# Performance work log

Measured on AMD Instinct MI355X. Metric: run time of the kernel, lower is better.

## Reference

```python
import jax, jax.numpy as jnp
import numpy as np

EMBED_DIM = 1024
NUM_HEADS = 16
HEAD_DIM = EMBED_DIM // NUM_HEADS
EPS = 1e-6


def setup_inputs() -> dict:
    key = jax.random.key(0)
    ks = jax.random.split(key, 10)
    B, S, D = 4, 2048, EMBED_DIM
    def xavier(k, shape):
        fan_in, fan_out = shape[1], shape[0]
        limit = float(np.sqrt(6.0 / (fan_in + fan_out)))
        return jax.random.uniform(k, shape, jnp.float32, -limit, limit)
    return {
        "x": jax.random.normal(ks[0], (B, S, D), jnp.float32),
        "ln_gamma": jnp.ones((D,), jnp.float32),
        "ln_beta": jnp.zeros((D,), jnp.float32),
        "Wq": xavier(ks[1], (D, D)), "bq": jnp.zeros((D,), jnp.float32),
        "Wk": xavier(ks[2], (D, D)), "bk": jnp.zeros((D,), jnp.float32),
        "Wv": xavier(ks[3], (D, D)), "bv": jnp.zeros((D,), jnp.float32),
        "Wo": xavier(ks[4], (D, D)), "bo": jnp.zeros((D,), jnp.float32),
    }


def reference(x, ln_gamma, ln_beta, Wq, bq, Wk, bk, Wv, bv, Wo, bo):
    B, S, D = x.shape
    # Pre-LayerNorm
    mu = jnp.mean(x, axis=-1, keepdims=True)
    var = jnp.mean((x - mu) ** 2, axis=-1, keepdims=True)
    xn = (x - mu) / jnp.sqrt(var + EPS) * ln_gamma + ln_beta
    # QKV projections (torch Linear: y = x @ W.T + b)
    def split_heads(t):  # [B,S,D] -> [B,H,S,hd]
        return t.reshape(B, S, NUM_HEADS, HEAD_DIM).transpose(0, 2, 1, 3)
    q = split_heads(xn @ Wq.T + bq)
    k = split_heads(xn @ Wk.T + bk)
    v = split_heads(xn @ Wv.T + bv)
    scale = 1.0 / jnp.sqrt(jnp.float32(HEAD_DIM))
    scores = jnp.einsum("bhqd,bhkd->bhqk", q, k) * scale
    probs = jax.nn.softmax(scores, axis=-1)  # dropout is identity (eval)
    ctx = jnp.einsum("bhqk,bhkd->bhqd", probs, v)
    ctx = ctx.transpose(0, 2, 1, 3).reshape(B, S, D)
    out = ctx @ Wo.T + bo  # proj dropout identity (eval)
    return out
```

## Files before the change

### kernel.cpp

```cpp
#include <hip/hip_runtime.h>
#include <hip/hip_bf16.h>
#include <stdint.h>

typedef __bf16 bf16x8 __attribute__((ext_vector_type(8)));
typedef short short8 __attribute__((ext_vector_type(8)));
typedef float f32x4 __attribute__((ext_vector_type(4)));

#define LOG2E 1.44269504088896340736f

__device__ inline void gload_lds16(const void* g, void* l) {
  __builtin_amdgcn_global_load_lds((const __attribute__((address_space(1))) void*)g,
                                   (__attribute__((address_space(3))) void*)l, 16, 0, 0);
}

__device__ inline unsigned short bf16_bits(float f) {
  return __builtin_bit_cast(unsigned short, __float2bfloat16(f));
}

__device__ inline float fast_exp2(float x) {
  return __builtin_amdgcn_exp2f(x);
}

__device__ inline uint32_t cvtpk_bf16(float lo, float hi) {
  uint32_t d;
  asm("v_cvt_pk_bf16_f32 %0, %1, %2" : "=v"(d) : "v"(lo), "v"(hi));
  return d;
}
__device__ inline void plswap32(uint32_t& a, uint32_t& b) {
  asm("v_permlane32_swap_b32 %0, %1" : "+v"(a), "+v"(b));
}
__device__ inline void plswap16(uint32_t& a, uint32_t& b) {
  asm("v_permlane16_swap_b32 %0, %1" : "+v"(a), "+v"(b));
}

__global__ __launch_bounds__(256) void prep_kernel(
    const float* __restrict__ x, const float* __restrict__ gamma,
    const float* __restrict__ beta, __hip_bfloat16* __restrict__ xn,
    const float* __restrict__ Wq, const float* __restrict__ Wk,
    const float* __restrict__ Wv, const float* __restrict__ Wo,
    __hip_bfloat16* __restrict__ Wqk, __hip_bfloat16* __restrict__ Wvb,
    __hip_bfloat16* __restrict__ Wob)
{
  const int t = threadIdx.x;
  if (blockIdx.x < 8192) {
    const int row = blockIdx.x;
    const float4 v = reinterpret_cast<const float4*>(x + (size_t)row * 1024)[t];
    float s = v.x + v.y + v.z + v.w;
    float q = v.x*v.x + v.y*v.y + v.z*v.z + v.w*v.w;
    #pragma unroll
    for (int off = 32; off >= 1; off >>= 1) {
      s += __shfl_xor(s, off);
      q += __shfl_xor(q, off);
    }
    __shared__ float ls[4], lq[4];
    const int wave = t >> 6, lane = t & 63;
    if (lane == 0) { ls[wave] = s; lq[wave] = q; }
    __syncthreads();
    s = ls[0] + ls[1] + ls[2] + ls[3];
    q = lq[0] + lq[1] + lq[2] + lq[3];
    const float mean = s * (1.0f/1024.0f);
    const float var  = q * (1.0f/1024.0f) - mean*mean;
    const float rstd = rsqrtf(var + 1e-6f);
    const float4 gm = reinterpret_cast<const float4*>(gamma)[t];
    const float4 bt = reinterpret_cast<const float4*>(beta)[t];
    ushort4 o;
    o.x = bf16_bits((v.x - mean)*rstd*gm.x + bt.x);
    o.y = bf16_bits((v.y - mean)*rstd*gm.y + bt.y);
    o.z = bf16_bits((v.z - mean)*rstd*gm.z + bt.z);
    o.w = bf16_bits((v.w - mean)*rstd*gm.w + bt.w);
    reinterpret_cast<ushort4*>(xn + (size_t)row*1024)[t] = o;
  } else {
    const int cb = blockIdx.x - 8192;
    const int which = cb >> 10;
    const int i = (cb & 1023) * 256 + t;
    const float* src;
    __hip_bfloat16* dst;
    if (which == 0)      { src = Wq; dst = Wqk; }
    else if (which == 1) { src = Wk; dst = Wqk + 1024*1024; }
    else if (which == 2) { src = Wv; dst = Wvb; }
    else                 { src = Wo; dst = Wob; }
    const float4 v = reinterpret_cast<const float4*>(src)[i];
    ushort4 o;
    o.x = bf16_bits(v.x); o.y = bf16_bits(v.y);
    o.z = bf16_bits(v.z); o.w = bf16_bits(v.w);
    reinterpret_cast<ushort4*>(dst)[i] = o;
  }
}

template<int MODE>
__device__ __forceinline__ void gemm_body(
    const __hip_bfloat16* __restrict__ A,
    const __hip_bfloat16* __restrict__ B,
    int m0, int n0,
    const float* __restrict__ bias0,
    const float* __restrict__ bias1,
    void* __restrict__ C0,
    void* __restrict__ C1,
    __hip_bfloat16* Al, __hip_bfloat16* Bl)
{
  constexpr int K = 1024;
  const int t = threadIdx.x;
  const int wave = t >> 6, lane = t & 63;
  const int li = lane & 15, g = lane >> 4;
  const int wm = (wave >> 1) * 64, wn = (wave & 1) * 64;

  const int srow = t >> 3;
  const int scb_e = ((((t & 7) * 16) ^ ((srow & 7) << 4)) >> 1);
  const __hip_bfloat16* ga = A + (size_t)(m0 + srow) * K + scb_e;
  const __hip_bfloat16* gb = B + (size_t)(n0 + srow) * K + scb_e;

  const int swz = (li & 7) << 4;
  const int rd0 = (((g*16)      ^ swz) >> 1);
  const int rd1 = (((g*16 + 64) ^ swz) >> 1);

  f32x4 acc[4][4] = {};

  for (int kt = 0; kt < K; kt += 64) {
    #pragma unroll
    for (int i = 0; i < 4; ++i) {
      gload_lds16(ga + (size_t)(i*32)*K + kt, Al + i*2048 + t*8);
      gload_lds16(gb + (size_t)(i*32)*K + kt, Bl + i*2048 + t*8);
    }
    __syncthreads();
    bf16x8 af[4][2], bfr[4][2];
    #pragma unroll
    for (int mi = 0; mi < 4; ++mi) {
      af[mi][0] = *reinterpret_cast<const bf16x8*>(&Al[(wm + mi*16 + li)*64 + rd0]);
      af[mi][1] = *reinterpret_cast<const bf16x8*>(&Al[(wm + mi*16 + li)*64 + rd1]);
    }
    #pragma unroll
    for (int ni = 0; ni < 4; ++ni) {
      bfr[ni][0] = *reinterpret_cast<const bf16x8*>(&Bl[(wn + ni*16 + li)*64 + rd0]);
      bfr[ni][1] = *reinterpret_cast<const bf16x8*>(&Bl[(wn + ni*16 + li)*64 + rd1]);
    }
    __builtin_amdgcn_s_setprio(1);
    #pragma unroll
    for (int mi = 0; mi < 4; ++mi)
      #pragma unroll
      for (int ni = 0; ni < 4; ++ni) {
        acc[mi][ni] = __builtin_amdgcn_mfma_f32_16x16x32_bf16(af[mi][0], bfr[ni][0], acc[mi][ni], 0, 0, 0);
        acc[mi][ni] = __builtin_amdgcn_mfma_f32_16x16x32_bf16(af[mi][1], bfr[ni][1], acc[mi][ni], 0, 0, 0);
      }
    __builtin_amdgcn_s_setprio(0);
    __syncthreads();
  }

  #pragma unroll
  for (int mi = 0; mi < 4; ++mi) {
    #pragma unroll
    for (int ni = 0; ni < 4; ++ni) {
      #pragma unroll
      for (int r = 0; r < 4; ++r) {
        const int grow = m0 + wm + mi*16 + g*4 + r;
        const int gcol = n0 + wn + ni*16 + li;
        float v = acc[mi][ni][r];
        if constexpr (MODE == 0) {
          const int b = grow >> 11, ss = grow & 2047;
          if (gcol < 1024) {
            v = (v + bias0[gcol]) * (0.125f * LOG2E);
            const int h = gcol >> 6, d = gcol & 63;
            ((__hip_bfloat16*)C0)[(((size_t)(b*16 + h))*2048 + ss)*64 + d] = __float2bfloat16(v);
          } else {
            const int c2 = gcol - 1024;
            v = v + bias1[c2];
            const int h = c2 >> 6, d = c2 & 63;
            ((__hip_bfloat16*)C1)[(((size_t)(b*16 + h))*2048 + ss)*64 + d] = __float2bfloat16(v);
          }
        } else if constexpr (MODE == 1) {
          v += bias0[grow];
          ((__hip_bfloat16*)C0)[(size_t)grow*8192 + gcol] = __float2bfloat16(v);
        } else {
          v += bias0[gcol];
          ((float*)C0)[(size_t)grow*1024 + gcol] = v;
        }
      }
    }
  }
}

__global__ __launch_bounds__(256) void qkv_gemm(
    const __hip_bfloat16* __restrict__ xn,
    const __hip_bfloat16* __restrict__ Wqk,
    const __hip_bfloat16* __restrict__ Wvb,
    const float* __restrict__ bq, const float* __restrict__ bk,
    const float* __restrict__ bv,
    __hip_bfloat16* __restrict__ Qb, __hip_bfloat16* __restrict__ Kb,
    __hip_bfloat16* __restrict__ Vt)
{
  __shared__ __align__(16) __hip_bfloat16 Al[128*64];
  __shared__ __align__(16) __hip_bfloat16 Bl[128*64];
  const int lin = blockIdx.x;
  const int wg  = (lin & 7) * 192 + (lin >> 3);
  if (wg < 1024) {
    const int m0 = (wg >> 4) * 128, n0 = (wg & 15) * 128;
    gemm_body<0>(xn, Wqk, m0, n0, bq, bk, Qb, Kb, Al, Bl);
  } else {
    const int w2 = wg - 1024;
    const int m0 = (w2 & 7) * 128, n0 = (w2 >> 3) * 128;
    gemm_body<1>(Wvb, xn, m0, n0, bv, nullptr, Vt, nullptr, Al, Bl);
  }
}

__global__ __launch_bounds__(256) void out_gemm(
    const __hip_bfloat16* __restrict__ A,
    const __hip_bfloat16* __restrict__ B,
    const float* __restrict__ bias,
    float* __restrict__ C)
{
  __shared__ __align__(16) __hip_bfloat16 Al[128*64];
  __shared__ __align__(16) __hip_bfloat16 Bl[128*64];
  const int lin = blockIdx.x;
  const int wg  = (lin & 7) * 64 + (lin >> 3);
  const int m0 = (wg >> 3) * 128, n0 = (wg & 7) * 128;
  gemm_body<2>(A, B, m0, n0, bias, nullptr, C, nullptr, Al, Bl);
}

__global__ __launch_bounds__(512, 8) void attn_kernel(
    const __hip_bfloat16* __restrict__ Q,
    const __hip_bfloat16* __restrict__ K,
    const __hip_bfloat16* __restrict__ Vt,
    __hip_bfloat16* __restrict__ ctx)
{
  const int t = threadIdx.x, wave = t >> 6, lane = t & 63;
  const int li = lane & 15, g = lane >> 4;

  const int lin = blockIdx.x;
  const int wg  = (lin & 7) * 128 + (lin >> 3);
  const int bh  = wg >> 4, qt = wg & 15;
  const int b = bh >> 4, h = bh & 15;
  const int qbase = qt * 128 + wave * 16;

  __shared__ __align__(16) __hip_bfloat16 Klds[2][4096];
  __shared__ __align__(16) __hip_bfloat16 Vlds[2][4096];

  const bf16x8* Qv = reinterpret_cast<const bf16x8*>(Q + ((size_t)bh*2048 + qbase + li)*64 + g*8);
  const bf16x8 aQ0 = Qv[0], aQ1 = Qv[4];

  const short8 ones_s = { 0x3F80, 0x3F80, 0x3F80, 0x3F80, 0x3F80, 0x3F80, 0x3F80, 0x3F80 };
  const bf16x8 ones = __builtin_bit_cast(bf16x8, ones_s);

  f32x4 acc[4] = {};
  f32x4 acc_l = {};

  const __hip_bfloat16* Kbh = K + (size_t)bh*2048*64;
  const __hip_bfloat16* Vbh = Vt + (size_t)h*64*8192 + b*2048;

  const int row0 = t >> 3;
  const int scb_e = ((((t & 7) * 16) ^ ((row0 & 7) << 4)) >> 1);

  const int krd0 = (li*128 + ((g*16)      ^ ((li & 7) << 4))) >> 1;
  const int krd1 = (li*128 + ((g*16 + 64) ^ ((li & 7) << 4))) >> 1;

  gload_lds16(Kbh + (size_t)row0*64 + scb_e,        &Klds[0][t*8]);
  gload_lds16(Vbh + (size_t)row0*8192 + scb_e,      &Vlds[0][t*8]);
  gload_lds16(Kbh + (size_t)(64+row0)*64 + scb_e,   &Klds[1][t*8]);
  gload_lds16(Vbh + (size_t)row0*8192 + 64 + scb_e, &Vlds[1][t*8]);
  asm volatile("s_waitcnt vmcnt(2)" ::: "memory");
  __builtin_amdgcn_sched_barrier(0);
  __builtin_amdgcn_s_barrier();

  const __hip_bfloat16* kSrc = Kbh + (size_t)(128 + row0)*64 + scb_e;
  const __hip_bfloat16* vSrc = Vbh + (size_t)row0*8192 + 128 + scb_e;

  for (int it = 0; it < 32; ++it) {
    const int cur = it & 1;
    const __hip_bfloat16* Kc = Klds[cur];
    const __hip_bfloat16* Vc = Vlds[cur];

    f32x4 s[4] = {};
    __builtin_amdgcn_s_setprio(1);
    #pragma unroll
    for (int nt = 0; nt < 4; ++nt) {
      const bf16x8 k0 = *reinterpret_cast<const bf16x8*>(&Kc[nt*1024 + krd0]);
      const bf16x8 k1 = *reinterpret_cast<const bf16x8*>(&Kc[nt*1024 + krd1]);
      s[nt] = __builtin_amdgcn_mfma_f32_16x16x32_bf16(k0, aQ0, s[nt], 0, 0, 0);
      s[nt] = __builtin_amdgcn_mfma_f32_16x16x32_bf16(k1, aQ1, s[nt], 0, 0, 0);
    }
    __builtin_amdgcn_s_setprio(0);

    #pragma unroll
    for (int nt = 0; nt < 4; ++nt)
      #pragma unroll
      for (int r = 0; r < 4; ++r)
        s[nt][r] = fast_exp2(s[nt][r]);

    union U8 { uint32_t w[4]; bf16x8 v; };
    bf16x8 aP0, aP1;
    {
      uint32_t c[4][2];
      #pragma unroll
      for (int nt = 0; nt < 4; ++nt) {
        c[nt][0] = cvtpk_bf16(s[nt][0], s[nt][1]);
        c[nt][1] = cvtpk_bf16(s[nt][2], s[nt][3]);
      }
      uint32_t x0 = c[0][0], y0 = c[1][0], x1 = c[0][1], y1 = c[1][1];
      plswap32(x0, y0); plswap32(x1, y1);
      plswap16(x0, y0); plswap16(x1, y1);
      U8 u0; u0.w[0] = x0; u0.w[1] = x1; u0.w[2] = y0; u0.w[3] = y1;
      aP0 = u0.v;
      uint32_t x2 = c[2][0], y2 = c[3][0], x3 = c[2][1], y3 = c[3][1];
      plswap32(x2, y2); plswap32(x3, y3);
      plswap16(x2, y2); plswap16(x3, y3);
      U8 u1; u1.w[0] = x2; u1.w[1] = x3; u1.w[2] = y2; u1.w[3] = y3;
      aP1 = u1.v;
    }

    __builtin_amdgcn_s_setprio(1);
    #pragma unroll
    for (int dt = 0; dt < 4; ++dt) {
      const bf16x8 v0 = *reinterpret_cast<const bf16x8*>(&Vc[dt*1024 + krd0]);
      const bf16x8 v1 = *reinterpret_cast<const bf16x8*>(&Vc[dt*1024 + krd1]);
      acc[dt] = __builtin_amdgcn_mfma_f32_16x16x32_bf16(v0, aP0, acc[dt], 0, 0, 0);
      acc[dt] = __builtin_amdgcn_mfma_f32_16x16x32_bf16(v1, aP1, acc[dt], 0, 0, 0);
    }
    acc_l = __builtin_amdgcn_mfma_f32_16x16x32_bf16(ones, aP0, acc_l, 0, 0, 0);
    acc_l = __builtin_amdgcn_mfma_f32_16x16x32_bf16(ones, aP1, acc_l, 0, 0, 0);
    __builtin_amdgcn_s_setprio(0);

    if (it < 31) {
      __builtin_amdgcn_s_barrier();
      if (it < 30) {
        gload_lds16(kSrc, &Klds[cur][t*8]);
        gload_lds16(vSrc, &Vlds[cur][t*8]);
        kSrc += 64*64;
        vSrc += 64;
        asm volatile("s_waitcnt vmcnt(2)" ::: "memory");
      } else {
        asm volatile("s_waitcnt vmcnt(0)" ::: "memory");
      }
      __builtin_amdgcn_sched_barrier(0);
      __builtin_amdgcn_s_barrier();
    }
  }

  const float inv = 1.0f / acc_l[0];

  __hip_bfloat16* cp = ctx + ((size_t)(b*2048 + qbase))*1024 + h*64;
  #pragma unroll
  for (int dt = 0; dt < 4; ++dt) {
    ushort4 o;
    o.x = bf16_bits(acc[dt][0] * inv);
    o.y = bf16_bits(acc[dt][1] * inv);
    o.z = bf16_bits(acc[dt][2] * inv);
    o.w = bf16_bits(acc[dt][3] * inv);
    *reinterpret_cast<ushort4*>(&cp[(size_t)li*1024 + dt*16 + g*4]) = o;
  }
}

extern "C" void kernel_launch(void* const* d_in, const int* in_sizes, int n_in,
                              void* d_out, int out_size, void* d_ws, size_t ws_size,
                              hipStream_t stream)
{
  const float* x  = (const float*)d_in[0];
  const float* g  = (const float*)d_in[1];
  const float* be = (const float*)d_in[2];
  const float* Wq = (const float*)d_in[3];
  const float* bq = (const float*)d_in[4];
  const float* Wk = (const float*)d_in[5];
  const float* bk = (const float*)d_in[6];
  const float* Wv = (const float*)d_in[7];
  const float* bv = (const float*)d_in[8];
  const float* Wo = (const float*)d_in[9];
  const float* bo = (const float*)d_in[10];
  float* out = (float*)d_out;

  char* ws = (char*)d_ws;
  __hip_bfloat16* xn  = (__hip_bfloat16*)(ws);
  __hip_bfloat16* Wqk = (__hip_bfloat16*)(ws + 16777216);
  __hip_bfloat16* Wvb = (__hip_bfloat16*)(ws + 20971520);
  __hip_bfloat16* Wob = (__hip_bfloat16*)(ws + 23068672);
  __hip_bfloat16* Qb  = (__hip_bfloat16*)(ws + 25165824);
  __hip_bfloat16* Kb  = (__hip_bfloat16*)(ws + 41943040);
  __hip_bfloat16* Vt  = (__hip_bfloat16*)(ws + 58720256);
  __hip_bfloat16* ctx = (__hip_bfloat16*)(ws + 75497472);

  prep_kernel<<<12288, 256, 0, stream>>>(x, g, be, xn, Wq, Wk, Wv, Wo, Wqk, Wvb, Wob);
  qkv_gemm<<<1536, 256, 0, stream>>>(xn, Wqk, Wvb, bq, bk, bv, Qb, Kb, Vt);
  attn_kernel<<<1024, 512, 0, stream>>>(Qb, Kb, Vt, ctx);
  out_gemm<<<512, 256, 0, stream>>>(ctx, Wob, bo, out);
}
```

Baseline: 189.0 us.

## Use 64x128 thin GEMM tiles for V and output projections; unroll attention loop

Adds a thin GEMM body with 64-row tiles (each wave covers 64x32) for the V projection and the output projection. This doubles the number of workgroups (1536 to 2048 for QKV, 512 to 1024 for the output GEMM) to fill the GPU's compute units better. The attention main loop is manually unrolled by two so the double-buffer index and branches become compile-time constant. Smaller tiles lower per-block arithmetic intensity and increase global/LDS traffic.

Measured after the change: 224.1 us. 18.6% more time.

```diff
diff --git a/kernel.cpp b/kernel.cpp
--- a/kernel.cpp
+++ b/kernel.cpp
@@ -87,15 +87,12 @@
   }
 }
 
-template<int MODE>
-__device__ __forceinline__ void gemm_body(
+__device__ __forceinline__ void gemm_body128(
     const __hip_bfloat16* __restrict__ A,
     const __hip_bfloat16* __restrict__ B,
     int m0, int n0,
-    const float* __restrict__ bias0,
-    const float* __restrict__ bias1,
-    void* __restrict__ C0,
-    void* __restrict__ C1,
+    const float* __restrict__ bq, const float* __restrict__ bk,
+    __hip_bfloat16* __restrict__ Qb, __hip_bfloat16* __restrict__ Kb,
     __hip_bfloat16* Al, __hip_bfloat16* Bl)
 {
   constexpr int K = 1024;
@@ -154,24 +151,94 @@
         const int grow = m0 + wm + mi*16 + g*4 + r;
         const int gcol = n0 + wn + ni*16 + li;
         float v = acc[mi][ni][r];
-        if constexpr (MODE == 0) {
-          const int b = grow >> 11, ss = grow & 2047;
-          if (gcol < 1024) {
-            v = (v + bias0[gcol]) * (0.125f * LOG2E);
-            const int h = gcol >> 6, d = gcol & 63;
-            ((__hip_bfloat16*)C0)[(((size_t)(b*16 + h))*2048 + ss)*64 + d] = __float2bfloat16(v);
-          } else {
-            const int c2 = gcol - 1024;
-            v = v + bias1[c2];
-            const int h = c2 >> 6, d = c2 & 63;
-            ((__hip_bfloat16*)C1)[(((size_t)(b*16 + h))*2048 + ss)*64 + d] = __float2bfloat16(v);
-          }
-        } else if constexpr (MODE == 1) {
-          v += bias0[grow];
-          ((__hip_bfloat16*)C0)[(size_t)grow*8192 + gcol] = __float2bfloat16(v);
+        const int b = grow >> 11, ss = grow & 2047;
+        if (gcol < 1024) {
+          v = (v + bq[gcol]) * (0.125f * LOG2E);
+          const int h = gcol >> 6, d = gcol & 63;
+          Qb[(((size_t)(b*16 + h))*2048 + ss)*64 + d] = __float2bfloat16(v);
         } else {
-          v += bias0[gcol];
-          ((float*)C0)[(size_t)grow*1024 + gcol] = v;
+          const int c2 = gcol - 1024;
+          v = v + bk[c2];
+          const int h = c2 >> 6, d = c2 & 63;
+          Kb[(((size_t)(b*16 + h))*2048 + ss)*64 + d] = __float2bfloat16(v);
+        }
+      }
+    }
+  }
+}
+
+template<int MODE>
+__device__ __forceinline__ void gemm_body_thin(
+    const __hip_bfloat16* __restrict__ A,
+    const __hip_bfloat16* __restrict__ B,
+    int m0, int n0,
+    const float* __restrict__ bias,
+    void* __restrict__ C,
+    __hip_bfloat16* Al, __hip_bfloat16* Bl)
+{
+  constexpr int K = 1024;
+  const int t = threadIdx.x;
+  const int wave = t >> 6, lane = t & 63;
+  const int li = lane & 15, g = lane >> 4;
+  const int wn = wave * 32;
+
+  const int srow = t >> 3;
+  const int scb_e = ((((t & 7) * 16) ^ ((srow & 7) << 4)) >> 1);
+  const __hip_bfloat16* ga = A + (size_t)(m0 + srow) * K + scb_e;
+  const __hip_bfloat16* gb = B + (size_t)(n0 + srow) * K + scb_e;
+
+  const int swz = (li & 7) << 4;
+  const int rd0 = (((g*16)      ^ swz) >> 1);
+  const int rd1 = (((g*16 + 64) ^ swz) >> 1);
+
+  f32x4 acc[4][2] = {};
+
+  for (int kt = 0; kt < K; kt += 64) {
+    #pragma unroll
+    for (int i = 0; i < 2; ++i)
+      gload_lds16(ga + (size_t)(i*32)*K + kt, Al + i*2048 + t*8);
+    #pragma unroll
+    for (int i = 0; i < 4; ++i)
+      gload_lds16(gb + (size_t)(i*32)*K + kt, Bl + i*2048 + t*8);
+    __syncthreads();
+    bf16x8 af[4][2], bfr[2][2];
+    #pragma unroll
+    for (int mi = 0; mi < 4; ++mi) {
+      af[mi][0] = *reinterpret_cast<const bf16x8*>(&Al[(mi*16 + li)*64 + rd0]);
+      af[mi][1] = *reinterpret_cast<const bf16x8*>(&Al[(mi*16 + li)*64 + rd1]);
+    }
+    #pragma unroll
+    for (int ni = 0; ni < 2; ++ni) {
+      bfr[ni][0] = *reinterpret_cast<const bf16x8*>(&Bl[(wn + ni*16 + li)*64 + rd0]);
+      bfr[ni][1] = *reinterpret_cast<const bf16x8*>(&Bl[(wn + ni*16 + li)*64 + rd1]);
+    }
+    __builtin_amdgcn_s_setprio(1);
+    #pragma unroll
+    for (int mi = 0; mi < 4; ++mi)
+      #pragma unroll
+      for (int ni = 0; ni < 2; ++ni) {
+        acc[mi][ni] = __builtin_amdgcn_mfma_f32_16x16x32_bf16(af[mi][0], bfr[ni][0], acc[mi][ni], 0, 0, 0);
+        acc[mi][ni] = __builtin_amdgcn_mfma_f32_16x16x32_bf16(af[mi][1], bfr[ni][1], acc[mi][ni], 0, 0, 0);
+      }
+    __builtin_amdgcn_s_setprio(0);
+    __syncthreads();
+  }
+
+  #pragma unroll
+  for (int mi = 0; mi < 4; ++mi) {
+    #pragma unroll
+    for (int ni = 0; ni < 2; ++ni) {
+      #pragma unroll
+      for (int r = 0; r < 4; ++r) {
+        const int grow = m0 + mi*16 + g*4 + r;
+        const int gcol = n0 + wn + ni*16 + li;
+        float v = acc[mi][ni][r];
+        if constexpr (MODE == 1) {
+          v += bias[grow];
+          ((__hip_bfloat16*)C)[(size_t)grow*8192 + gcol] = __float2bfloat16(v);
+        } else {
+          v += bias[gcol];
+          ((float*)C)[(size_t)grow*1024 + gcol] = v;
         }
       }
     }
@@ -190,14 +257,14 @@
   __shared__ __align__(16) __hip_bfloat16 Al[128*64];
   __shared__ __align__(16) __hip_bfloat16 Bl[128*64];
   const int lin = blockIdx.x;
-  const int wg  = (lin & 7) * 192 + (lin >> 3);
+  const int wg  = (lin & 7) * 256 + (lin >> 3);
   if (wg < 1024) {
     const int m0 = (wg >> 4) * 128, n0 = (wg & 15) * 128;
-    gemm_body<0>(xn, Wqk, m0, n0, bq, bk, Qb, Kb, Al, Bl);
+    gemm_body128(xn, Wqk, m0, n0, bq, bk, Qb, Kb, Al, Bl);
   } else {
     const int w2 = wg - 1024;
-    const int m0 = (w2 & 7) * 128, n0 = (w2 >> 3) * 128;
-    gemm_body<1>(Wvb, xn, m0, n0, bv, nullptr, Vt, nullptr, Al, Bl);
+    const int m0 = (w2 >> 6) * 64, n0 = (w2 & 63) * 128;
+    gemm_body_thin<1>(Wvb, xn, m0, n0, bv, Vt, Al, Bl);
   }
 }
 
@@ -207,12 +274,12 @@
     const float* __restrict__ bias,
     float* __restrict__ C)
 {
-  __shared__ __align__(16) __hip_bfloat16 Al[128*64];
+  __shared__ __align__(16) __hip_bfloat16 Al[64*64];
   __shared__ __align__(16) __hip_bfloat16 Bl[128*64];
   const int lin = blockIdx.x;
-  const int wg  = (lin & 7) * 64 + (lin >> 3);
-  const int m0 = (wg >> 3) * 128, n0 = (wg & 7) * 128;
-  gemm_body<2>(A, B, m0, n0, bias, nullptr, C, nullptr, Al, Bl);
+  const int wg  = (lin & 7) * 128 + (lin >> 3);
+  const int m0 = (wg >> 3) * 64, n0 = (wg & 7) * 128;
+  gemm_body_thin<2>(A, B, m0, n0, bias, C, Al, Bl);
 }
 
 __global__ __launch_bounds__(512, 8) void attn_kernel(
@@ -251,22 +318,7 @@
   const int krd0 = (li*128 + ((g*16)      ^ ((li & 7) << 4))) >> 1;
   const int krd1 = (li*128 + ((g*16 + 64) ^ ((li & 7) << 4))) >> 1;
 
-  gload_lds16(Kbh + (size_t)row0*64 + scb_e,        &Klds[0][t*8]);
-  gload_lds16(Vbh + (size_t)row0*8192 + scb_e,      &Vlds[0][t*8]);
-  gload_lds16(Kbh + (size_t)(64+row0)*64 + scb_e,   &Klds[1][t*8]);
-  gload_lds16(Vbh + (size_t)row0*8192 + 64 + scb_e, &Vlds[1][t*8]);
-  asm volatile("s_waitcnt vmcnt(2)" ::: "memory");
-  __builtin_amdgcn_sched_barrier(0);
-  __builtin_amdgcn_s_barrier();
-
-  const __hip_bfloat16* kSrc = Kbh + (size_t)(128 + row0)*64 + scb_e;
-  const __hip_bfloat16* vSrc = Vbh + (size_t)row0*8192 + 128 + scb_e;
-
-  for (int it = 0; it < 32; ++it) {
-    const int cur = it & 1;
-    const __hip_bfloat16* Kc = Klds[cur];
-    const __hip_bfloat16* Vc = Vlds[cur];
-
+  auto compute = [&](const __hip_bfloat16* Kc, const __hip_bfloat16* Vc) {
     f32x4 s[4] = {};
     __builtin_amdgcn_s_setprio(1);
     #pragma unroll
@@ -316,22 +368,43 @@
     acc_l = __builtin_amdgcn_mfma_f32_16x16x32_bf16(ones, aP0, acc_l, 0, 0, 0);
     acc_l = __builtin_amdgcn_mfma_f32_16x16x32_bf16(ones, aP1, acc_l, 0, 0, 0);
     __builtin_amdgcn_s_setprio(0);
-
-    if (it < 31) {
-      __builtin_amdgcn_s_barrier();
-      if (it < 30) {
-        gload_lds16(kSrc, &Klds[cur][t*8]);
-        gload_lds16(vSrc, &Vlds[cur][t*8]);
-        kSrc += 64*64;
-        vSrc += 64;
-        asm volatile("s_waitcnt vmcnt(2)" ::: "memory");
-      } else {
-        asm volatile("s_waitcnt vmcnt(0)" ::: "memory");
-      }
-      __builtin_amdgcn_sched_barrier(0);
-      __builtin_amdgcn_s_barrier();
-    }
-  }
+  };
+
+  gload_lds16(Kbh + (size_t)row0*64 + scb_e,        &Klds[0][t*8]);
+  gload_lds16(Vbh + (size_t)row0*8192 + scb_e,      &Vlds[0][t*8]);
+  gload_lds16(Kbh + (size_t)(64+row0)*64 + scb_e,   &Klds[1][t*8]);
+  gload_lds16(Vbh + (size_t)row0*8192 + 64 + scb_e, &Vlds[1][t*8]);
+  asm volatile("s_waitcnt vmcnt(2)" ::: "memory");
+  __builtin_amdgcn_sched_barrier(0);
+  __builtin_amdgcn_s_barrier();
+
+  const __hip_bfloat16* kSrc = Kbh + (size_t)(128 + row0)*64 + scb_e;
+  const __hip_bfloat16* vSrc = Vbh + (size_t)row0*8192 + 128 + scb_e;
+
+  for (int i = 0; i < 15; ++i) {
+    compute(Klds[0], Vlds[0]);
+    __builtin_amdgcn_s_barrier();
+    gload_lds16(kSrc, &Klds[0][t*8]);
+    gload_lds16(vSrc, &Vlds[0][t*8]);
+    kSrc += 64*64; vSrc += 64;
+    asm volatile("s_waitcnt vmcnt(2)" ::: "memory");
+    __builtin_amdgcn_sched_barrier(0);
+    __builtin_amdgcn_s_barrier();
+    compute(Klds[1], Vlds[1]);
+    __builtin_amdgcn_s_barrier();
+    gload_lds16(kSrc, &Klds[1][t*8]);
+    gload_lds16(vSrc, &Vlds[1][t*8]);
+    kSrc += 64*64; vSrc += 64;
+    asm volatile("s_waitcnt vmcnt(2)" ::: "memory");
+    __builtin_amdgcn_sched_barrier(0);
+    __builtin_amdgcn_s_barrier();
+  }
+  compute(Klds[0], Vlds[0]);
+  __builtin_amdgcn_s_barrier();
+  asm volatile("s_waitcnt vmcnt(0)" ::: "memory");
+  __builtin_amdgcn_sched_barrier(0);
+  __builtin_amdgcn_s_barrier();
+  compute(Klds[1], Vlds[1]);
 
   const float inv = 1.0f / acc_l[0];
 
@@ -375,7 +448,7 @@
   __hip_bfloat16* ctx = (__hip_bfloat16*)(ws + 75497472);
 
   prep_kernel<<<12288, 256, 0, stream>>>(x, g, be, xn, Wq, Wk, Wv, Wo, Wqk, Wvb, Wob);
-  qkv_gemm<<<1536, 256, 0, stream>>>(xn, Wqk, Wvb, bq, bk, bv, Qb, Kb, Vt);
+  qkv_gemm<<<2048, 256, 0, stream>>>(xn, Wqk, Wvb, bq, bk, bv, Qb, Kb, Vt);
   attn_kernel<<<1024, 512, 0, stream>>>(Qb, Kb, Vt, ctx);
-  out_gemm<<<512, 256, 0, stream>>>(ctx, Wob, bo, out);
-}
+  out_gemm<<<1024, 256, 0, stream>>>(ctx, Wob, bo, out);
+}
```
